# Optimization experiments

Hardware: AMD Instinct MI355X
Metric: run time of the kernel (lower is better)

Reference implementation:

```python
import jax, jax.numpy as jnp
import numpy as np

EMBED_DIM = 768
NUM_HEADS = 12
HEAD_DIM = EMBED_DIM // NUM_HEADS
SCALE = HEAD_DIM ** -0.5
B, N = 8, 1024


def setup_inputs() -> dict:
    key = jax.random.key(0)
    ks = jax.random.split(key, 5)
    return {
        "x": jax.random.normal(ks[0], (B, N, EMBED_DIM), dtype=jnp.float32),
        "qkv_w": jax.random.normal(ks[1], (3 * EMBED_DIM, EMBED_DIM), dtype=jnp.float32) * 0.02,
        "qkv_b": jax.random.normal(ks[2], (3 * EMBED_DIM,), dtype=jnp.float32) * 0.02,
        "proj_w": jax.random.normal(ks[3], (EMBED_DIM, EMBED_DIM), dtype=jnp.float32) * 0.02,
        "proj_b": jax.random.normal(ks[4], (EMBED_DIM,), dtype=jnp.float32) * 0.02,
    }


def reference(x, qkv_w, qkv_b, proj_w, proj_b):
    b, n, c = x.shape
    h, hd = NUM_HEADS, HEAD_DIM
    # QKV projection: [b,n,3c]
    qkv = jnp.einsum("bnc,dc->bnd", x, qkv_w) + qkv_b
    qkv = qkv.reshape(b, n, 3, h, hd).transpose(2, 0, 3, 1, 4)  # [3,b,h,n,hd]
    q, k, v = qkv[0], qkv[1], qkv[2]
    # scaled dot-product attention (eager path; dropout is identity in eval)
    attn = jnp.einsum("bhqd,bhkd->bhqk", q, k) * SCALE
    attn = jax.nn.softmax(attn, axis=-1)
    out = jnp.einsum("bhqk,bhkd->bhqd", attn, v)  # [b,h,n,hd]
    out = out.transpose(0, 2, 1, 3).reshape(b, n, c)
    # output projection
    return jnp.einsum("bnc,dc->bnd", out, proj_w) + proj_b
```

## Files before the change

### kernel.cpp

```cpp
#include <hip/hip_runtime.h>
#include <hip/hip_bf16.h>

typedef __attribute__((ext_vector_type(4))) float f32x4;
typedef __attribute__((ext_vector_type(8))) short short8;
typedef unsigned short u16;

#define MFMA(a, b, c) __builtin_amdgcn_mfma_f32_16x16x32_bf16((a), (b), (c), 0, 0, 0)

#define WAITVM_BAR(N) do {                                          \
    asm volatile("s_waitcnt vmcnt(" #N ")" ::: "memory");           \
    __builtin_amdgcn_s_barrier();                                   \
    __builtin_amdgcn_sched_barrier(0);                              \
} while (0)
#define BAR2() do {                                                 \
    __builtin_amdgcn_sched_barrier(0);                              \
    __builtin_amdgcn_s_barrier();                                   \
    __builtin_amdgcn_sched_barrier(0);                              \
} while (0)

static constexpr int EMBED = 768;
static constexpr int NH = 12;
static constexpr int HD = 64;
static constexpr int BATCH = 8;
static constexpr int SEQ = 1024;

__device__ __forceinline__ u16 f2bu(float f) {
    __hip_bfloat16 h = __float2bfloat16(f);
    u16 u; __builtin_memcpy(&u, &h, 2); return u;
}
__device__ __forceinline__ float exp2a(float x) {
    float r; asm("v_exp_f32 %0, %1" : "=v"(r) : "v"(x)); return r;
}
__device__ __forceinline__ unsigned cvt_pk_bf16(float lo, float hi) {
    unsigned r; asm("v_cvt_pk_bf16_f32 %0, %1, %2" : "=v"(r) : "v"(lo), "v"(hi)); return r;
}
__device__ __forceinline__ float max3f(float a, float b, float c) {
    return fmaxf(fmaxf(a, b), c);
}
__device__ __forceinline__ void swap32(unsigned& a, unsigned& b) {
    asm volatile("v_permlane32_swap_b32 %0, %1" : "+v"(a), "+v"(b));
}
__device__ __forceinline__ void swap16(unsigned& a, unsigned& b) {
    asm volatile("v_permlane16_swap_b32 %0, %1" : "+v"(a), "+v"(b));
}
__device__ __forceinline__ short8 mk8(unsigned w0, unsigned w1, unsigned w2, unsigned w3) {
    union { unsigned u[4]; short8 s; } c;
    c.u[0] = w0; c.u[1] = w1; c.u[2] = w2; c.u[3] = w3;
    return c.s;
}

__global__ void cvt_bf16_k(const float* __restrict__ in, u16* __restrict__ out, int n) {
    int i = (blockIdx.x * blockDim.x + threadIdx.x) * 4;
    if (i >= n) return;
    float4 v = *reinterpret_cast<const float4*>(in + i);
    ushort4 o;
    o.x = f2bu(v.x); o.y = f2bu(v.y); o.z = f2bu(v.z); o.w = f2bu(v.w);
    *reinterpret_cast<ushort4*>(out + i) = o;
}

template <int EPI>
__global__ __launch_bounds__(256)
void gemm_bt_k(const u16* __restrict__ A, const u16* __restrict__ Bw,
               const float* __restrict__ bias,
               u16* __restrict__ q_out, u16* __restrict__ k_out,
               u16* __restrict__ vt_out, float* __restrict__ f_out)
{
    __shared__ __attribute__((aligned(16))) char smem[65536];
    const int tid  = threadIdx.x;
    const int wave = tid >> 6, lane = tid & 63;
    const int hi   = lane >> 4, l15 = lane & 15;
    const int wr   = wave >> 1, wc = wave & 1;
    const int bm   = blockIdx.x, bn = blockIdx.y;

    f32x4 acc[4][4] = {};

    const size_t arow0 = (size_t)bm * 128;
    const size_t brow0 = (size_t)bn * 128;

    auto stage = [&](int buf, int kt) {
        char* Ab = smem + buf * 32768;
        char* Bb = Ab + 16384;
#pragma unroll
        for (int c = 0; c < 4; ++c) {
            int ck   = c * 4 + wave;
            int p    = ck * 1024 + lane * 16;
            int row  = p >> 7;
            int pcol = (p & 127) ^ ((row & 7) << 4);
            const u16* srcA = A  + (arow0 + row) * EMBED + kt + (pcol >> 1);
            const u16* srcB = Bw + (brow0 + row) * EMBED + kt + (pcol >> 1);
            __builtin_amdgcn_global_load_lds((const __attribute__((address_space(1))) void*)srcA,
                                             (__attribute__((address_space(3))) void*)(Ab + ck * 1024), 16, 0, 0);
            __builtin_amdgcn_global_load_lds((const __attribute__((address_space(1))) void*)srcB,
                                             (__attribute__((address_space(3))) void*)(Bb + ck * 1024), 16, 0, 0);
        }
    };

    auto comp = [&](const char* Ab, const char* Bb) {
#pragma unroll
        for (int kk = 0; kk < 2; ++kk) {
            short8 af[4], bf[4];
#pragma unroll
            for (int mi = 0; mi < 4; ++mi) {
                int R  = wr * 64 + mi * 16 + l15;
                int Cb = kk * 64 + hi * 16;
                af[mi] = *reinterpret_cast<const short8*>(Ab + R * 128 + (Cb ^ ((R & 7) << 4)));
            }
#pragma unroll
            for (int ni = 0; ni < 4; ++ni) {
                int R  = wc * 64 + ni * 16 + l15;
                int Cb = kk * 64 + hi * 16;
                bf[ni] = *reinterpret_cast<const short8*>(Bb + R * 128 + (Cb ^ ((R & 7) << 4)));
            }
#pragma unroll
            for (int mi = 0; mi < 4; ++mi)
#pragma unroll
                for (int ni = 0; ni < 4; ++ni)
                    acc[mi][ni] = MFMA(af[mi], bf[ni], acc[mi][ni]);
        }
    };

    const char* A0 = smem;
    const char* B0 = smem + 16384;
    const char* A1 = smem + 32768;
    const char* B1 = smem + 49152;

    stage(0, 0);
#pragma unroll
    for (int tt = 0; tt < 5; ++tt) {
        stage(1, (2 * tt + 1) * 64);
        WAITVM_BAR(8);
        comp(A0, B0);
        BAR2();
        stage(0, (2 * tt + 2) * 64);
        WAITVM_BAR(8);
        comp(A1, B1);
        BAR2();
    }
    stage(1, 11 * 64);
    WAITVM_BAR(8);
    comp(A0, B0);
    BAR2();
    WAITVM_BAR(0);
    comp(A1, B1);

#pragma unroll
    for (int mi = 0; mi < 4; ++mi) {
        int crow0 = bm * 128 + wr * 64 + mi * 16 + hi * 4;
#pragma unroll
        for (int ni = 0; ni < 4; ++ni) {
            int ccol = bn * 128 + wc * 64 + ni * 16 + l15;
            float bv = bias[ccol];
            if constexpr (EPI == 0) {
                int which = ccol / 768;
                int rem   = ccol - which * 768;
                int hh = rem >> 6, hd = rem & 63;
                int bb = crow0 >> 10, nn0 = crow0 & 1023;
                size_t bh = (size_t)(bb * NH + hh);
                if (which == 2) {
                    uint2 pk;
                    pk.x = cvt_pk_bf16(acc[mi][ni][0] + bv, acc[mi][ni][1] + bv);
                    pk.y = cvt_pk_bf16(acc[mi][ni][2] + bv, acc[mi][ni][3] + bv);
                    *reinterpret_cast<uint2*>(&vt_out[(bh * HD + hd) * SEQ + nn0]) = pk;
                } else if (which == 0) {
#pragma unroll
                    for (int r = 0; r < 4; ++r)
                        q_out[(bh * SEQ + nn0 + r) * HD + hd] =
                            f2bu((acc[mi][ni][r] + bv) * 0.18033688f);
                } else {
#pragma unroll
                    for (int r = 0; r < 4; ++r)
                        k_out[(bh * SEQ + nn0 + r) * HD + hd] = f2bu(acc[mi][ni][r] + bv);
                }
            } else {
#pragma unroll
                for (int r = 0; r < 4; ++r)
                    f_out[(size_t)(crow0 + r) * EMBED + ccol] = acc[mi][ni][r] + bv;
            }
        }
    }
}

__global__ __launch_bounds__(512, 6)
void attn_k(const u16* __restrict__ Q, const u16* __restrict__ K,
            const u16* __restrict__ Vt, u16* __restrict__ AO)
{
    __shared__ __attribute__((aligned(16))) u16 kls[2][4096];
    __shared__ __attribute__((aligned(16))) u16 vls[2][4096];

    const int tid = threadIdx.x;
    const int w   = tid >> 6, lane = tid & 63;
    const int hi  = lane >> 4, l15 = lane & 15;
    const int f   = blockIdx.x;
    const int xcd = f & 7, i = f >> 3;
    const int bh  = xcd * 12 + (i % 12);
    const int q0w = (i / 12) * 128 + w * 16;

    const u16* Qh = Q  + (size_t)bh * SEQ * HD;
    const u16* Kh = K  + (size_t)bh * SEQ * HD;
    const u16* Vh = Vt + (size_t)bh * HD * SEQ;

    const int sp    = w * 1024 + lane * 16;
    const int srow  = sp >> 7;
    const int scolb = (sp & 127) ^ ((srow & 7) << 4);
    const u16* kbase = Kh + (size_t)srow * HD + (scolb >> 1);
    const u16* vbase = Vh + (size_t)srow * SEQ + (scolb >> 1);

    auto stage = [&](int buf, int t) {
        __builtin_amdgcn_global_load_lds(
            (const __attribute__((address_space(1))) void*)(kbase + (size_t)t * 64 * HD),
            (__attribute__((address_space(3))) void*)(&kls[buf][w * 512]), 16, 0, 0);
        __builtin_amdgcn_global_load_lds(
            (const __attribute__((address_space(1))) void*)(vbase + (size_t)t * 64),
            (__attribute__((address_space(3))) void*)(&vls[buf][w * 512]), 16, 0, 0);
    };

    stage(0, 0);

    short8 qf[2];
#pragma unroll
    for (int dh = 0; dh < 2; ++dh)
        qf[dh] = *reinterpret_cast<const short8*>(
            Qh + (size_t)(q0w + l15) * HD + dh * 32 + hi * 8);

    f32x4 accO[4] = {};
    float m = -1e30f, lp = 0.f;

    auto tile = [&](const u16* Kb, const u16* Vb) {
        f32x4 st[4] = {};
        __builtin_amdgcn_s_setprio(1);
#pragma unroll
        for (int kb = 0; kb < 4; ++kb) {
            int R  = kb * 16 + l15;
            int sw = (R & 7) << 4;
            short8 kf0 = *reinterpret_cast<const short8*>(Kb + R * 64 + (((hi * 16) ^ sw) >> 1));
            short8 kf1 = *reinterpret_cast<const short8*>(Kb + R * 64 + (((64 + hi * 16) ^ sw) >> 1));
            st[kb] = MFMA(kf0, qf[0], st[kb]);
            st[kb] = MFMA(kf1, qf[1], st[kb]);
        }
        __builtin_amdgcn_s_setprio(0);

        float t0 = max3f(st[0][0], st[0][1], st[0][2]);
        float t1 = max3f(st[0][3], st[1][0], st[1][1]);
        float t2 = max3f(st[1][2], st[1][3], st[2][0]);
        float t3 = max3f(st[2][1], st[2][2], st[2][3]);
        float t4 = max3f(st[3][0], st[3][1], st[3][2]);
        float tm = fmaxf(max3f(t0, t1, t2), max3f(t3, t4, st[3][3]));
        tm = fmaxf(tm, __shfl_xor(tm, 16, 64));
        tm = fmaxf(tm, __shfl_xor(tm, 32, 64));
        if (!__all(tm <= m + 8.f)) {
            float mn = fmaxf(m, tm);
            float sc = exp2a(m - mn);
            m = mn;
            lp *= sc;
#pragma unroll
            for (int db = 0; db < 4; ++db)
#pragma unroll
                for (int r = 0; r < 4; ++r) accO[db][r] *= sc;
        }

        unsigned X[4][2];
#pragma unroll
        for (int kb = 0; kb < 4; ++kb) {
            float e0 = exp2a(st[kb][0] - m);
            float e1 = exp2a(st[kb][1] - m);
            float e2 = exp2a(st[kb][2] - m);
            float e3 = exp2a(st[kb][3] - m);
            lp += (e0 + e1) + (e2 + e3);
            X[kb][0] = cvt_pk_bf16(e0, e1);
            X[kb][1] = cvt_pk_bf16(e2, e3);
        }

        unsigned a0 = X[0][0], b0 = X[1][0];
        swap32(a0, b0); swap16(a0, b0);
        unsigned a1 = X[0][1], b1 = X[1][1];
        swap32(a1, b1); swap16(a1, b1);
        unsigned a2 = X[2][0], b2 = X[3][0];
        swap32(a2, b2); swap16(a2, b2);
        unsigned a3 = X[2][1], b3 = X[3][1];
        swap32(a3, b3); swap16(a3, b3);
        short8 pa0 = mk8(a0, a1, b0, b1);
        short8 pa1 = mk8(a2, a3, b2, b3);

        __builtin_amdgcn_s_setprio(1);
#pragma unroll
        for (int db = 0; db < 4; ++db) {
            int R  = db * 16 + l15;
            int sw = (R & 7) << 4;
            short8 vf0 = *reinterpret_cast<const short8*>(Vb + R * 64 + (((hi * 16) ^ sw) >> 1));
            short8 vf1 = *reinterpret_cast<const short8*>(Vb + R * 64 + (((64 + hi * 16) ^ sw) >> 1));
            accO[db] = MFMA(vf0, pa0, accO[db]);
            accO[db] = MFMA(vf1, pa1, accO[db]);
        }
        __builtin_amdgcn_s_setprio(0);
    };

    for (int tt = 0; tt < 7; ++tt) {
        stage(1, 2 * tt + 1);
        WAITVM_BAR(2);
        tile(kls[0], vls[0]);
        BAR2();
        stage(0, 2 * tt + 2);
        WAITVM_BAR(2);
        tile(kls[1], vls[1]);
        BAR2();
    }
    stage(1, 15);
    WAITVM_BAR(2);
    tile(kls[0], vls[0]);
    BAR2();
    WAITVM_BAR(0);
    tile(kls[1], vls[1]);

    lp += __shfl_xor(lp, 16, 64);
    lp += __shfl_xor(lp, 32, 64);
    float linv = 1.f / lp;
    const int bb = bh / NH, hh = bh - bb * NH;
    size_t rowb = ((size_t)bb * SEQ + q0w + l15) * EMBED + hh * HD;
#pragma unroll
    for (int db = 0; db < 4; ++db) {
        float o0 = accO[db][0] * linv, o1 = accO[db][1] * linv;
        float o2 = accO[db][2] * linv, o3 = accO[db][3] * linv;
        uint2 pkd;
        pkd.x = cvt_pk_bf16(o0, o1);
        pkd.y = cvt_pk_bf16(o2, o3);
        *reinterpret_cast<uint2*>(&AO[rowb + db * 16 + hi * 4]) = pkd;
    }
}

extern "C" void kernel_launch(void* const* d_in, const int* in_sizes, int n_in,
                              void* d_out, int out_size, void* d_ws, size_t ws_size,
                              hipStream_t stream)
{
    const float* x      = (const float*)d_in[0];
    const float* qkv_w  = (const float*)d_in[1];
    const float* qkv_b  = (const float*)d_in[2];
    const float* proj_w = (const float*)d_in[3];
    const float* proj_b = (const float*)d_in[4];
    float* out = (float*)d_out;

    char* ws = (char*)d_ws;
    u16* xb  = (u16*)(ws);
    u16* wb  = (u16*)(ws + 12582912);
    u16* pw  = (u16*)(ws + 16121856);
    u16* qb  = (u16*)(ws + 17301504);
    u16* kb  = (u16*)(ws + 29884416);
    u16* vt  = (u16*)(ws + 42467328);
    u16* ao  = (u16*)(ws + 55050240);

    cvt_bf16_k<<<6144, 256, 0, stream>>>(x,      xb, BATCH * SEQ * EMBED);
    cvt_bf16_k<<<1728, 256, 0, stream>>>(qkv_w,  wb, 3 * EMBED * EMBED);
    cvt_bf16_k<<<576,  256, 0, stream>>>(proj_w, pw, EMBED * EMBED);

    gemm_bt_k<0><<<dim3(64, 18), 256, 0, stream>>>(xb, wb, qkv_b, qb, kb, vt, nullptr);
    attn_k<<<768, 512, 0, stream>>>(qb, kb, vt, ao);
    gemm_bt_k<1><<<dim3(64, 6), 256, 0, stream>>>(ao, pw, proj_b, nullptr, nullptr, nullptr, out);
}
```

Baseline: 107.1 us.

## Triple-buffer attention K/V staging and merge fp32-to-bf16 conversion launches

The attention kernel moves from double to triple buffering of K/V tiles in LDS. Each step now needs one barrier instead of two, and the load for tile t+2 is issued before computing tile t, so global loads have more lead time. Separately, the three fp32-to-bf16 conversion kernels become one launch that picks its source by index range, cutting launch overhead. The cost is more LDS per block (48KB), which may lower occupancy relative to the launch_bounds target of 6. With a single barrier, there is also a possible race where a slow wave is still reading the buffer being overwritten.

```diff
diff --git a/kernel.cpp b/kernel.cpp
--- a/kernel.cpp
+++ b/kernel.cpp
@@ -49,13 +49,22 @@
     return c.s;
 }
 
-__global__ void cvt_bf16_k(const float* __restrict__ in, u16* __restrict__ out, int n) {
+__global__ void cvt_all_k(const float* __restrict__ x, const float* __restrict__ w1,
+                          const float* __restrict__ w2,
+                          u16* __restrict__ xb, u16* __restrict__ wb, u16* __restrict__ pw) {
+    const int n1 = BATCH * SEQ * EMBED;
+    const int n2 = 3 * EMBED * EMBED;
+    const int n3 = EMBED * EMBED;
     int i = (blockIdx.x * blockDim.x + threadIdx.x) * 4;
-    if (i >= n) return;
-    float4 v = *reinterpret_cast<const float4*>(in + i);
+    const float* src; u16* dst;
+    if (i < n1)            { src = x  + i;             dst = xb + i; }
+    else if (i < n1 + n2)  { src = w1 + (i - n1);      dst = wb + (i - n1); }
+    else if (i < n1+n2+n3) { src = w2 + (i - n1 - n2); dst = pw + (i - n1 - n2); }
+    else return;
+    float4 v = *reinterpret_cast<const float4*>(src);
     ushort4 o;
     o.x = f2bu(v.x); o.y = f2bu(v.y); o.z = f2bu(v.z); o.w = f2bu(v.w);
-    *reinterpret_cast<ushort4*>(out + i) = o;
+    *reinterpret_cast<ushort4*>(dst) = o;
 }
 
 template <int EPI>
@@ -184,8 +193,8 @@
 void attn_k(const u16* __restrict__ Q, const u16* __restrict__ K,
             const u16* __restrict__ Vt, u16* __restrict__ AO)
 {
-    __shared__ __attribute__((aligned(16))) u16 kls[2][4096];
-    __shared__ __attribute__((aligned(16))) u16 vls[2][4096];
+    __shared__ __attribute__((aligned(16))) u16 kls[3][4096];
+    __shared__ __attribute__((aligned(16))) u16 vls[3][4096];
 
     const int tid = threadIdx.x;
     const int w   = tid >> 6, lane = tid & 63;
@@ -205,22 +214,24 @@
     const u16* kbase = Kh + (size_t)srow * HD + (scolb >> 1);
     const u16* vbase = Vh + (size_t)srow * SEQ + (scolb >> 1);
 
-    auto stage = [&](int buf, int t) {
+    auto stage = [&](u16* kdst, u16* vdst, int t) {
         __builtin_amdgcn_global_load_lds(
             (const __attribute__((address_space(1))) void*)(kbase + (size_t)t * 64 * HD),
-            (__attribute__((address_space(3))) void*)(&kls[buf][w * 512]), 16, 0, 0);
+            (__attribute__((address_space(3))) void*)(kdst + w * 512), 16, 0, 0);
         __builtin_amdgcn_global_load_lds(
             (const __attribute__((address_space(1))) void*)(vbase + (size_t)t * 64),
-            (__attribute__((address_space(3))) void*)(&vls[buf][w * 512]), 16, 0, 0);
-    };
-
-    stage(0, 0);
+            (__attribute__((address_space(3))) void*)(vdst + w * 512), 16, 0, 0);
+    };
 
     short8 qf[2];
 #pragma unroll
     for (int dh = 0; dh < 2; ++dh)
         qf[dh] = *reinterpret_cast<const short8*>(
             Qh + (size_t)(q0w + l15) * HD + dh * 32 + hi * 8);
+    __builtin_amdgcn_sched_barrier(0);
+
+    stage(kls[0], vls[0], 0);
+    stage(kls[1], vls[1], 1);
 
     f32x4 accO[4] = {};
     float m = -1e30f, lp = 0.f;
@@ -294,22 +305,24 @@
         __builtin_amdgcn_s_setprio(0);
     };
 
-    for (int tt = 0; tt < 7; ++tt) {
-        stage(1, 2 * tt + 1);
-        WAITVM_BAR(2);
-        tile(kls[0], vls[0]);
-        BAR2();
-        stage(0, 2 * tt + 2);
-        WAITVM_BAR(2);
-        tile(kls[1], vls[1]);
-        BAR2();
+    auto one = [&](const u16* Kc, const u16* Vc, u16* Ks, u16* Vs, int tn, bool ds) {
+        asm volatile("s_waitcnt vmcnt(2)" ::: "memory");
+        __builtin_amdgcn_s_barrier();
+        __builtin_amdgcn_sched_barrier(0);
+        if (ds) stage(Ks, Vs, tn);
+        tile(Kc, Vc);
+        __builtin_amdgcn_sched_barrier(0);
+    };
+
+    for (int g = 0; g < 5; ++g) {
+        one(kls[0], vls[0], kls[2], vls[2], 3 * g + 2, true);
+        one(kls[1], vls[1], kls[0], vls[0], 3 * g + 3, 3 * g + 3 <= 15);
+        one(kls[2], vls[2], kls[1], vls[1], 3 * g + 4, 3 * g + 4 <= 15);
     }
-    stage(1, 15);
-    WAITVM_BAR(2);
+    asm volatile("s_waitcnt vmcnt(0)" ::: "memory");
+    __builtin_amdgcn_s_barrier();
+    __builtin_amdgcn_sched_barrier(0);
     tile(kls[0], vls[0]);
-    BAR2();
-    WAITVM_BAR(0);
-    tile(kls[1], vls[1]);
 
     lp += __shfl_xor(lp, 16, 64);
     lp += __shfl_xor(lp, 32, 64);
@@ -347,9 +360,7 @@
     u16* vt  = (u16*)(ws + 42467328);
     u16* ao  = (u16*)(ws + 55050240);
 
-    cvt_bf16_k<<<6144, 256, 0, stream>>>(x,      xb, BATCH * SEQ * EMBED);
-    cvt_bf16_k<<<1728, 256, 0, stream>>>(qkv_w,  wb, 3 * EMBED * EMBED);
-    cvt_bf16_k<<<576,  256, 0, stream>>>(proj_w, pw, EMBED * EMBED);
+    cvt_all_k<<<8448, 256, 0, stream>>>(x, qkv_w, proj_w, xb, wb, pw);
 
     gemm_bt_k<0><<<dim3(64, 18), 256, 0, stream>>>(xb, wb, qkv_b, qb, kb, vt, nullptr);
     attn_k<<<768, 512, 0, stream>>>(qb, kb, vt, ao);
```

New measurement: 103.8 us. 1.03x faster.
